# Kernel tuning notes

Measured on AMD Instinct MI355X. Metric: run time of the kernel, lower is better.

## Reference

```python
import jax, jax.numpy as jnp
import numpy as np

N_NODES = 50000
N_EDGES = 500000
DIM = 128
N_REL = 51
N_LAYERS = 4
B, K = 1024, 32
EPS = 1e-6


def setup_inputs() -> dict:
    key = jax.random.key(0)
    ks = jax.random.split(key, 10)
    x0 = jax.random.normal(ks[0], (N_NODES, DIM), jnp.float32)
    edge_index = jax.random.randint(ks[1], (2, N_EDGES), 0, N_NODES, dtype=jnp.int32)
    edge_type = jax.random.randint(ks[2], (N_EDGES,), 0, N_REL, dtype=jnp.int32)
    edge_weight = jnp.ones((N_EDGES,), jnp.float32)
    rel_w = jax.random.normal(ks[3], (N_LAYERS, N_REL, DIM), jnp.float32) * 0.1
    lin_w = jax.random.normal(ks[4], (N_LAYERS, 13 * DIM, DIM), jnp.float32) * (1.0 / np.sqrt(13 * DIM))
    lin_b = jnp.zeros((N_LAYERS, DIM), jnp.float32)
    ln_g = jnp.ones((N_LAYERS, DIM), jnp.float32)
    ln_b = jnp.zeros((N_LAYERS, DIM), jnp.float32)
    query_w = jax.random.normal(ks[5], (N_REL, DIM), jnp.float32) * 0.1
    src = jax.random.randint(ks[6], (B, K), 0, N_NODES, dtype=jnp.int32)
    rel = jax.random.randint(ks[7], (B, K), 0, N_REL, dtype=jnp.int32)
    dst = jax.random.randint(ks[8], (B, K), 0, N_NODES, dtype=jnp.int32)
    return dict(x0=x0, edge_index=edge_index, edge_type=edge_type, edge_weight=edge_weight,
                rel_w=rel_w, lin_w=lin_w, lin_b=lin_b, ln_g=ln_g, ln_b=ln_b,
                query_w=query_w, src=src, rel=rel, dst=dst)


def _rgcn_forward(x0, edge_weight, rel_w, lin_w, lin_b, ln_g, ln_b, query_w,
                  edge_index, edge_type, src, rel, dst):
    s, d = edge_index[0], edge_index[1]
    # in-degree (each node also gets an implicit boundary self-message)
    deg = jax.ops.segment_sum(jnp.ones((N_EDGES,), x0.dtype), d, num_segments=N_NODES)
    degree_out = deg[:, None] + 1.0  # [N,1]
    scale = jnp.log(degree_out)
    scale = scale / scale.mean()
    # PNA degree scalers: identity, amplification, attenuation  [N,3]
    scales = jnp.concatenate([jnp.ones_like(scale), scale, 1.0 / jnp.clip(scale, 1e-2)], axis=-1)

    x = x0
    for l in range(N_LAYERS):
        # distmult message per edge: [E, D]
        msg = x[s] * rel_w[l][edge_type] * edge_weight[:, None]
        # aggregate with boundary (x0) as self-loop message
        sum_m = jax.ops.segment_sum(msg, d, num_segments=N_NODES) + x0
        sum_sq = jax.ops.segment_sum(msg * msg, d, num_segments=N_NODES) + x0 * x0
        mx = jnp.maximum(jax.ops.segment_max(msg, d, num_segments=N_NODES), x0)
        mn = jnp.minimum(jax.ops.segment_min(msg, d, num_segments=N_NODES), x0)
        mean = sum_m / degree_out
        sq_mean = sum_sq / degree_out
        std = jnp.sqrt(jnp.clip(sq_mean - mean * mean, EPS, None))
        feats = jnp.stack([mean, mx, mn, std], axis=-2)        # [N,4,D]
        out = (feats[:, None, :, :] * scales[:, :, None, None]).reshape(N_NODES, 12 * DIM)
        out = jnp.concatenate([out, x], axis=-1) @ lin_w[l] + lin_b[l]  # [N,D]
        # layer norm
        mu = out.mean(-1, keepdims=True)
        var = out.var(-1, keepdims=True)
        out = (out - mu) / jnp.sqrt(var + 1e-5) * ln_g[l] + ln_b[l]
        out = jax.nn.relu(out)
        x = out + x  # short cut (same shapes)

    # distmult scoring over (src, rel, dst) triples: [B, K]
    return (x[src] * query_w[rel] * x[dst]).sum(-1)


def reference(x0, edge_index, edge_type, edge_weight, rel_w, lin_w, lin_b,
              ln_g, ln_b, query_w, src, rel, dst):
    return _rgcn_forward(x0, edge_weight, rel_w, lin_w, lin_b, ln_g, ln_b, query_w,
                         edge_index, edge_type, src, rel, dst)
```

## Files before the change

kernel.cpp:

```cpp
#include <hip/hip_runtime.h>
#include <math.h>

#define NNODES 50000
#define NEDGES 500000
#define DIM 128
#define NREL 51
#define NLAYERS 4
#define NTRIPLES (1024*32)
#define KDIM 1664
#define TILE_US 4096
#define NBLK 196

typedef float f2 __attribute__((ext_vector_type(2)));
typedef float f32x4 __attribute__((ext_vector_type(4)));
typedef short bf16x8 __attribute__((ext_vector_type(8)));

static __device__ __forceinline__ ushort bf16_rne(float v) {
  unsigned u = __float_as_uint(v);
  unsigned r = (u + 0x7fffu + ((u >> 16) & 1u)) >> 16;
  return (ushort)r;
}
static __device__ __forceinline__ float bf16_f(ushort h) {
  return __uint_as_float(((unsigned)h) << 16);
}
static __device__ __forceinline__ f2 unpack_bf2(uint u) {
  f2 r;
  r.x = __uint_as_float(u << 16);
  r.y = __uint_as_float(u & 0xffff0000u);
  return r;
}
static __device__ __forceinline__ f2 fmax2(f2 a, f2 b) { f2 r; r.x = fmaxf(a.x,b.x); r.y = fmaxf(a.y,b.y); return r; }
static __device__ __forceinline__ f2 fmin2(f2 a, f2 b) { f2 r; r.x = fminf(a.x,b.x); r.y = fminf(a.y,b.y); return r; }

static __device__ __forceinline__ void gload_lds16(const void* g, void* l) {
  __builtin_amdgcn_global_load_lds(
      (const __attribute__((address_space(1))) unsigned int*)g,
      (__attribute__((address_space(3))) unsigned int*)l,
      16, 0, 0);
}


__global__ void deg_hist_k(const int* __restrict__ ei, int* __restrict__ deg) {
  int e = blockIdx.x * blockDim.x + threadIdx.x;
  if (e < NEDGES) atomicAdd(&deg[ei[NEDGES + e]], 1);
}

__global__ void logsum_k(const int* __restrict__ deg, float* __restrict__ acc) {
  int i = blockIdx.x * blockDim.x + threadIdx.x;
  float v = (i < NNODES) ? logf((float)(deg[i] + 1)) : 0.0f;
  #pragma unroll
  for (int m = 32; m >= 1; m >>= 1) v += __shfl_xor(v, m, 64);
  __shared__ float ws[4];
  int lane = threadIdx.x & 63, w = threadIdx.x >> 6;
  if (lane == 0) ws[w] = v;
  __syncthreads();
  if (threadIdx.x == 0) atomicAdd(acc, ws[0] + ws[1] + ws[2] + ws[3]);
}


__global__ __launch_bounds__(256) void blocksum_k(const int* __restrict__ deg,
                                                  int* __restrict__ bsum) {
  int idx = blockIdx.x * 256 + threadIdx.x;
  int v = (idx < NNODES) ? deg[idx] : 0;
  #pragma unroll
  for (int m = 32; m >= 1; m >>= 1) v += __shfl_xor(v, m, 64);
  __shared__ int ws[4];
  int lane = threadIdx.x & 63, w = threadIdx.x >> 6;
  if (lane == 0) ws[w] = v;
  __syncthreads();
  if (threadIdx.x == 0) bsum[blockIdx.x] = ws[0] + ws[1] + ws[2] + ws[3];
}

__global__ __launch_bounds__(256) void bscan_k(const int* __restrict__ bsum,
                                               int* __restrict__ bofs) {
  int t = threadIdx.x;
  int v = (t < NBLK) ? bsum[t] : 0;
  int lane = t & 63, w = t >> 6;
  int sc = v;
  #pragma unroll
  for (int off = 1; off < 64; off <<= 1) {
    int u = __shfl_up(sc, off, 64);
    if (lane >= off) sc += u;
  }
  __shared__ int ws[4];
  if (lane == 63) ws[w] = sc;
  __syncthreads();
  int wo = 0;
  for (int i = 0; i < w; ++i) wo += ws[i];
  if (t < NBLK) bofs[t] = wo + sc - v;
}

__global__ __launch_bounds__(256) void csr_offsets_k(const int* __restrict__ deg,
                                                     const int* __restrict__ bofs,
                                                     int* __restrict__ row_start,
                                                     int* __restrict__ cursor) {
  int t = threadIdx.x;
  int idx = blockIdx.x * 256 + t;
  int v = (idx < NNODES) ? deg[idx] : 0;
  int lane = t & 63, w = t >> 6;
  int sc = v;
  #pragma unroll
  for (int off = 1; off < 64; off <<= 1) {
    int u = __shfl_up(sc, off, 64);
    if (lane >= off) sc += u;
  }
  __shared__ int ws[4];
  if (lane == 63) ws[w] = sc;
  __syncthreads();
  int wo = 0;
  for (int i = 0; i < w; ++i) wo += ws[i];
  int excl = bofs[blockIdx.x] + wo + sc - v;
  if (idx < NNODES) {
    row_start[idx] = excl;
    cursor[idx] = excl;
    if (idx == NNODES - 1) row_start[NNODES] = excl + v;
  }
}

__global__ void scales_k(const int* __restrict__ deg, const float* __restrict__ logsum,
                         float* __restrict__ scales) {
  int i = blockIdx.x * blockDim.x + threadIdx.x;
  if (i >= NNODES) return;
  float mean = *logsum / (float)NNODES;
  float sc = logf((float)(deg[i] + 1)) / mean;
  scales[i*3 + 0] = 1.0f;
  scales[i*3 + 1] = sc;
  scales[i*3 + 2] = 1.0f / fmaxf(sc, 0.01f);
}

__global__ void scatter_k(const int* __restrict__ ei, const int* __restrict__ etype,
                          const float* __restrict__ ew, int* __restrict__ cursor,
                          int* __restrict__ s_srt, int* __restrict__ t_srt,
                          float* __restrict__ w_srt) {
  int e = blockIdx.x * blockDim.x + threadIdx.x;
  if (e >= NEDGES) return;
  int d = ei[NEDGES + e];
  int pos = atomicAdd(&cursor[d], 1);
  s_srt[pos] = ei[e];
  t_srt[pos] = etype[e];
  w_srt[pos] = ew[e];
}


__global__ void wsplit_k(const float* __restrict__ W, ushort* __restrict__ wt) {
  int id = blockIdx.x * blockDim.x + threadIdx.x;
  if (id >= NLAYERS * KDIM * DIM) return;
  int col = id & 127;
  int k = (id >> 7) % KDIM;
  int l = id / (KDIM * DIM);
  float v = W[(size_t)l * KDIM * DIM + (size_t)k * DIM + col];
  ushort h = bf16_rne(v);
  ushort lo = bf16_rne(v - bf16_f(h));
  int c = k >> 5, kk = k & 31;
  int by = col >> 6, ch = col & 63;
  int tidx = (c < 48) ? ((c & 15) * 3 + (c >> 4)) : c;
  size_t base = (size_t)(((size_t)l * 2 + by) * 52 + tidx) * TILE_US;
  int slot = (kk >> 3) ^ ((ch >> 1) & 3);
  int off = ch * 32 + (slot << 3) + (kk & 7);
  wt[base + off] = h;
  wt[base + 2048 + off] = lo;
}


__global__ void xsplit_k(const float* __restrict__ x, ushort* __restrict__ xh,
                         ushort* __restrict__ xl) {
  int id = blockIdx.x * blockDim.x + threadIdx.x;
  if (id >= NNODES * 64) return;
  f2 v = *(const f2*)(x + (size_t)id * 2);
  ushort h0 = bf16_rne(v.x), h1 = bf16_rne(v.y);
  ushort l0 = bf16_rne(v.x - bf16_f(h0)), l1 = bf16_rne(v.y - bf16_f(h1));
  ((uint*)xh)[id] = (uint)h0 | ((uint)h1 << 16);
  ((uint*)xl)[id] = (uint)l0 | ((uint)l1 << 16);
}


__global__ __launch_bounds__(256) void aggregate_k(
    const ushort* __restrict__ xh, const float* __restrict__ x0,
    const float* __restrict__ relw, const int* __restrict__ row_start,
    const int* __restrict__ s_srt, const int* __restrict__ t_srt,
    const float* __restrict__ w_srt,
    ushort* __restrict__ sh)
{
  int wid = blockIdx.x * 4 + (threadIdx.x >> 6);
  if (wid >= NNODES) return;
  int lane = threadIdx.x & 63;
  int j0 = lane * 2;
  int beg = row_start[wid], end = row_start[wid + 1];
  int deg = end - beg;
  f2 sum = {0.f, 0.f}, sq = {0.f, 0.f};
  f2 mx = {-INFINITY, -INFINITY}, mn = {INFINITY, INFINITY};

  int eidx = beg + lane;
  bool va = eidx < end;
  int   sv = va ? s_srt[eidx] : 0;
  int   tv = va ? t_srt[eidx] : 0;
  float wv = va ? w_srt[eidx] : 0.0f;

  int n = (deg < 64) ? deg : 64;
  int e = 0;
  for (; e + 4 <= n; e += 4) {
    int s0 = __shfl(sv, e, 64),     s1 = __shfl(sv, e + 1, 64);
    int s2 = __shfl(sv, e + 2, 64), s3 = __shfl(sv, e + 3, 64);
    int t0 = __shfl(tv, e, 64),     t1 = __shfl(tv, e + 1, 64);
    int t2 = __shfl(tv, e + 2, 64), t3 = __shfl(tv, e + 3, 64);
    float w0 = __shfl(wv, e, 64),     w1 = __shfl(wv, e + 1, 64);
    float w2 = __shfl(wv, e + 2, 64), w3 = __shfl(wv, e + 3, 64);
    f2 xa = unpack_bf2(*(const uint*)(xh + (size_t)s0 * DIM + j0));
    f2 xb = unpack_bf2(*(const uint*)(xh + (size_t)s1 * DIM + j0));
    f2 xc = unpack_bf2(*(const uint*)(xh + (size_t)s2 * DIM + j0));
    f2 xd = unpack_bf2(*(const uint*)(xh + (size_t)s3 * DIM + j0));
    f2 ra = *(const f2*)(relw + (size_t)t0 * DIM + j0);
    f2 rb = *(const f2*)(relw + (size_t)t1 * DIM + j0);
    f2 rc = *(const f2*)(relw + (size_t)t2 * DIM + j0);
    f2 rd = *(const f2*)(relw + (size_t)t3 * DIM + j0);
    f2 m0 = xa * ra * w0;
    f2 m1 = xb * rb * w1;
    f2 m2 = xc * rc * w2;
    f2 m3 = xd * rd * w3;
    sum += m0 + m1 + m2 + m3;
    sq += m0*m0 + m1*m1 + m2*m2 + m3*m3;
    mx = fmax2(fmax2(fmax2(mx, m0), fmax2(m1, m2)), m3);
    mn = fmin2(fmin2(fmin2(mn, m0), fmin2(m1, m2)), m3);
  }
  for (; e < n; ++e) {
    int s = __shfl(sv, e, 64);
    int ty = __shfl(tv, e, 64);
    float w = __shfl(wv, e, 64);
    f2 xs = unpack_bf2(*(const uint*)(xh + (size_t)s * DIM + j0));
    f2 rv = *(const f2*)(relw + (size_t)ty * DIM + j0);
    f2 m = xs * rv * w;
    sum += m; sq += m * m;
    mx = fmax2(mx, m); mn = fmin2(mn, m);
  }
  for (int ee = beg + 64; ee < end; ++ee) {
    int s = s_srt[ee]; int ty = t_srt[ee]; float w = w_srt[ee];
    f2 xs = unpack_bf2(*(const uint*)(xh + (size_t)s * DIM + j0));
    f2 rv = *(const f2*)(relw + (size_t)ty * DIM + j0);
    f2 m = xs * rv * w;
    sum += m; sq += m * m;
    mx = fmax2(mx, m); mn = fmin2(mn, m);
  }

  f2 x0v = *(const f2*)(x0 + (size_t)wid * DIM + j0);
  sum += x0v; sq += x0v * x0v;
  mx = fmax2(mx, x0v); mn = fmin2(mn, x0v);
  float dq = (float)(deg + 1);
  f2 mean = sum / dq;
  f2 sqm = sq / dq;
  f2 var = sqm - mean * mean;
  f2 sd; sd.x = sqrtf(fmaxf(var.x, 1e-6f)); sd.y = sqrtf(fmaxf(var.y, 1e-6f));
  f2 feats[4] = {mean, mx, mn, sd};
  size_t base = (size_t)wid * 512 + j0;
  #pragma unroll
  for (int f = 0; f < 4; ++f) {
    f2 v = feats[f];
    ushort h0 = bf16_rne(v.x), h1 = bf16_rne(v.y);
    *(uint*)(sh + base + f * 128) = (uint)h0 | ((uint)h1 << 16);
  }
}


__global__ __launch_bounds__(512, 2) void gemm_mfma_k(
    const ushort* __restrict__ sh,
    const ushort* __restrict__ xh, const ushort* __restrict__ xl,
    const float* __restrict__ scales, const ushort* __restrict__ wtl,
    float* __restrict__ Y)
{
  __shared__ ushort As[2 * TILE_US];
  __shared__ ushort Bs[2][3 * TILE_US];
  int t = threadIdx.x;
  int w = t >> 6, lane = t & 63;
  int lr = lane & 15, lk = lane >> 4;
  int wr = w >> 1, wcq = w & 1;
  int row0 = blockIdx.x * 128;
  int by = blockIdx.y;

  int sr = t >> 2, sq = t & 3;
  int an = row0 + sr; if (an >= NNODES) an = NNODES - 1;
  int aoff = sr * 32 + ((sq ^ ((sr >> 1) & 3)) << 3);

  f32x4 p0_00, p0_01, p0_10, p0_11;
  f32x4 p1_00, p1_01, p1_10, p1_11;
  f32x4 p2_00, p2_01, p2_10, p2_11;
  p0_00 = p0_01 = p0_10 = p0_11 = (f32x4){0.f,0.f,0.f,0.f};
  p1_00 = p1_01 = p1_10 = p1_11 = (f32x4){0.f,0.f,0.f,0.f};
  p2_00 = p2_01 = p2_10 = p2_11 = (f32x4){0.f,0.f,0.f,0.f};

  bf16x8 rh, rl;
  auto loadA = [&](int cp) {
    if (cp < 16) {
      rh = *(const bf16x8*)(sh + (size_t)an * 512 + cp * 32 + sq * 8);
    } else {
      rh = *(const bf16x8*)(xh + (size_t)an * 128 + (cp - 16) * 32 + sq * 8);
      rl = *(const bf16x8*)(xl + (size_t)an * 128 + (cp - 16) * 32 + sq * 8);
    }
  };
  auto issueB = [&](int cp, ushort* dst) {
    int tile0 = (cp < 16) ? cp * 3 : cp + 32;
    const char* src = (const char*)(wtl + ((size_t)by * 52 + tile0) * TILE_US);
    char* d = (char*)dst;
    gload_lds16(src + t * 16, d + t * 16);
    if (cp < 16) {
      gload_lds16(src + (512 + t) * 16, d + (512 + t) * 16);
      gload_lds16(src + (1024 + t) * 16, d + (1024 + t) * 16);
    }
  };

  issueB(0, Bs[0]);
  loadA(0);
  *(bf16x8*)(As + aoff) = rh;
  __syncthreads();

  int cur = 0;
  const int ar = wr * 32 + lr;
  const int aswz = ar * 32 + ((lk ^ ((ar >> 1) & 3)) << 3);
  const int br = wcq * 32 + lr;
  const int bswz = br * 32 + ((lk ^ ((br >> 1) & 3)) << 3);

#define LOADB(Btile)                                                               \
    const ushort* Bb = (Btile) + bswz;                                             \
    bf16x8 bh0 = *(const bf16x8*)(Bb);                                             \
    bf16x8 bl0 = *(const bf16x8*)(Bb + 2048);                                      \
    bf16x8 bh1 = *(const bf16x8*)(Bb + 512);                                       \
    bf16x8 bl1 = *(const bf16x8*)(Bb + 2048 + 512);

#define MFMA_S2(pa, pb, pc, pd, Btile)                                             \
  {                                                                                \
    LOADB(Btile)                                                                   \
    pa = __builtin_amdgcn_mfma_f32_16x16x32_bf16(ah0, bh0, pa, 0,0,0);             \
    pa = __builtin_amdgcn_mfma_f32_16x16x32_bf16(ah0, bl0, pa, 0,0,0);             \
    pb = __builtin_amdgcn_mfma_f32_16x16x32_bf16(ah0, bh1, pb, 0,0,0);             \
    pb = __builtin_amdgcn_mfma_f32_16x16x32_bf16(ah0, bl1, pb, 0,0,0);             \
    pc = __builtin_amdgcn_mfma_f32_16x16x32_bf16(ah1, bh0, pc, 0,0,0);             \
    pc = __builtin_amdgcn_mfma_f32_16x16x32_bf16(ah1, bl0, pc, 0,0,0);             \
    pd = __builtin_amdgcn_mfma_f32_16x16x32_bf16(ah1, bh1, pd, 0,0,0);             \
    pd = __builtin_amdgcn_mfma_f32_16x16x32_bf16(ah1, bl1, pd, 0,0,0);             \
  }

#define MFMA_S3(pa, pb, pc, pd, Btile)                                             \
  {                                                                                \
    LOADB(Btile)                                                                   \
    pa = __builtin_amdgcn_mfma_f32_16x16x32_bf16(ah0, bh0, pa, 0,0,0);             \
    pa = __builtin_amdgcn_mfma_f32_16x16x32_bf16(ah0, bl0, pa, 0,0,0);             \
    pa = __builtin_amdgcn_mfma_f32_16x16x32_bf16(al0, bh0, pa, 0,0,0);             \
    pb = __builtin_amdgcn_mfma_f32_16x16x32_bf16(ah0, bh1, pb, 0,0,0);             \
    pb = __builtin_amdgcn_mfma_f32_16x16x32_bf16(ah0, bl1, pb, 0,0,0);             \
    pb = __builtin_amdgcn_mfma_f32_16x16x32_bf16(al0, bh1, pb, 0,0,0);             \
    pc = __builtin_amdgcn_mfma_f32_16x16x32_bf16(ah1, bh0, pc, 0,0,0);             \
    pc = __builtin_amdgcn_mfma_f32_16x16x32_bf16(ah1, bl0, pc, 0,0,0);             \
    pc = __builtin_amdgcn_mfma_f32_16x16x32_bf16(al1, bh0, pc, 0,0,0);             \
    pd = __builtin_amdgcn_mfma_f32_16x16x32_bf16(ah1, bh1, pd, 0,0,0);             \
    pd = __builtin_amdgcn_mfma_f32_16x16x32_bf16(ah1, bl1, pd, 0,0,0);             \
    pd = __builtin_amdgcn_mfma_f32_16x16x32_bf16(al1, bh1, pd, 0,0,0);             \
  }

  for (int cp = 0; cp < 20; ++cp) {
    if (cp < 19) {
      issueB(cp + 1, Bs[cur ^ 1]);
      loadA(cp + 1);
    }
    const ushort* Ab = As + aswz;
    const ushort* Bcur = Bs[cur];
    if (cp < 16) {
      bf16x8 ah0 = *(const bf16x8*)(Ab);
      bf16x8 ah1 = *(const bf16x8*)(Ab + 512);
      MFMA_S2(p0_00, p0_01, p0_10, p0_11, Bcur);
      MFMA_S2(p1_00, p1_01, p1_10, p1_11, Bcur + TILE_US);
      MFMA_S2(p2_00, p2_01, p2_10, p2_11, Bcur + 2 * TILE_US);
    } else {
      bf16x8 ah0 = *(const bf16x8*)(Ab);
      bf16x8 al0 = *(const bf16x8*)(Ab + TILE_US);
      bf16x8 ah1 = *(const bf16x8*)(Ab + 512);
      bf16x8 al1 = *(const bf16x8*)(Ab + TILE_US + 512);
      MFMA_S3(p0_00, p0_01, p0_10, p0_11, Bcur);
    }
    __syncthreads();
    if (cp < 19) {
      *(bf16x8*)(As + aoff) = rh;
      if (cp + 1 >= 16) *(bf16x8*)(As + TILE_US + aoff) = rl;
    }
    cur ^= 1;
    __syncthreads();
  }
#undef MFMA_S2
#undef MFMA_S3
#undef LOADB

  int colg = by * 64 + wcq * 32;
  f32x4 q0[2][2] = {{p0_00, p0_01}, {p0_10, p0_11}};
  f32x4 q1[2][2] = {{p1_00, p1_01}, {p1_10, p1_11}};
  f32x4 q2[2][2] = {{p2_00, p2_01}, {p2_10, p2_11}};
  #pragma unroll
  for (int fr = 0; fr < 2; ++fr) {
    int rbase = row0 + wr * 32 + fr * 16 + lk * 4;
    #pragma unroll
    for (int q = 0; q < 4; ++q) {
      int r = rbase + q;
      int rc = (r < NNODES) ? r : (NNODES - 1);
      float s1 = scales[rc * 3 + 1];
      float s2 = scales[rc * 3 + 2];
      if (r < NNODES) {
        #pragma unroll
        for (int fc = 0; fc < 2; ++fc) {
          float o = q0[fr][fc][q] + s1 * q1[fr][fc][q] + s2 * q2[fr][fc][q];
          Y[(size_t)r * DIM + colg + fc * 16 + lr] = o;
        }
      }
    }
  }
}


__global__ __launch_bounds__(256) void ln_k(
    const float* __restrict__ Y, const float* __restrict__ bias,
    const float* __restrict__ gam, const float* __restrict__ bet,
    float* __restrict__ x, ushort* __restrict__ xh, ushort* __restrict__ xl)
{
  int wid = blockIdx.x * 4 + (threadIdx.x >> 6);
  if (wid >= NNODES) return;
  int lane = threadIdx.x & 63;
  int j0 = lane * 2;
  f2 v = *(const f2*)(Y + (size_t)wid * DIM + j0);
  f2 b = *(const f2*)(bias + j0);
  v += b;
  float s = v.x + v.y;
  float q = v.x * v.x + v.y * v.y;
  #pragma unroll
  for (int m = 1; m < 64; m <<= 1) { s += __shfl_xor(s, m, 64); q += __shfl_xor(q, m, 64); }
  float mu = s * (1.0f / 128.0f);
  float var = q * (1.0f / 128.0f) - mu * mu;
  float rstd = rsqrtf(var + 1e-5f);
  f2 g = *(const f2*)(gam + j0);
  f2 be = *(const f2*)(bet + j0);
  f2 o = (v - mu) * rstd * g + be;
  o.x = fmaxf(o.x, 0.f); o.y = fmaxf(o.y, 0.f);
  float* xp = x + (size_t)wid * DIM + j0;
  f2 xr = *(const f2*)xp;
  f2 res = o + xr;
  *(f2*)xp = res;
  ushort h0 = bf16_rne(res.x), h1 = bf16_rne(res.y);
  ushort l0 = bf16_rne(res.x - bf16_f(h0)), l1 = bf16_rne(res.y - bf16_f(h1));
  *(uint*)(xh + (size_t)wid * 128 + j0) = (uint)h0 | ((uint)h1 << 16);
  *(uint*)(xl + (size_t)wid * 128 + j0) = (uint)l0 | ((uint)l1 << 16);
}


__global__ __launch_bounds__(256) void score_k(
    const float* __restrict__ x, const float* __restrict__ qw,
    const int* __restrict__ src, const int* __restrict__ rel,
    const int* __restrict__ dst, float* __restrict__ out)
{
  int wid = blockIdx.x * 4 + (threadIdx.x >> 6);
  if (wid >= NTRIPLES) return;
  int lane = threadIdx.x & 63;
  int j0 = lane * 2;
  int s = src[wid], r = rel[wid], d = dst[wid];
  f2 xs = *(const f2*)(x  + (size_t)s * DIM + j0);
  f2 q  = *(const f2*)(qw + (size_t)r * DIM + j0);
  f2 xd = *(const f2*)(x  + (size_t)d * DIM + j0);
  float p = xs.x*q.x*xd.x + xs.y*q.y*xd.y;
  #pragma unroll
  for (int m = 32; m >= 1; m >>= 1) p += __shfl_xor(p, m, 64);
  if (lane == 0) out[wid] = p;
}


extern "C" void kernel_launch(void* const* d_in, const int* in_sizes, int n_in,
                              void* d_out, int out_size, void* d_ws, size_t ws_size,
                              hipStream_t stream) {
  const float* x0    = (const float*)d_in[0];
  const int*   ei    = (const int*)d_in[1];
  const int*   etyp  = (const int*)d_in[2];
  const float* ew    = (const float*)d_in[3];
  const float* rel_w = (const float*)d_in[4];
  const float* lin_w = (const float*)d_in[5];
  const float* lin_b = (const float*)d_in[6];
  const float* ln_g  = (const float*)d_in[7];
  const float* lnb   = (const float*)d_in[8];
  const float* qw    = (const float*)d_in[9];
  const int*   srcq  = (const int*)d_in[10];
  const int*   relq  = (const int*)d_in[11];
  const int*   dstq  = (const int*)d_in[12];
  float* out = (float*)d_out;

  char* ws = (char*)d_ws;
  size_t off = 0;
  auto alloc = [&](size_t bytes) -> void* {
    void* p = ws + off; off = (off + bytes + 255) & ~(size_t)255; return p;
  };
  int*    deg       = (int*)alloc((size_t)NNODES * 4);
  int*    row_start = (int*)alloc((size_t)(NNODES + 1) * 4);
  int*    cursor    = (int*)alloc((size_t)NNODES * 4);
  int*    bsum      = (int*)alloc((size_t)(NBLK + 1) * 4);
  int*    bofs      = (int*)alloc((size_t)(NBLK + 1) * 4);
  int*    s_srt     = (int*)alloc((size_t)NEDGES * 4);
  int*    t_srt     = (int*)alloc((size_t)NEDGES * 4);
  float*  w_srt     = (float*)alloc((size_t)NEDGES * 4);
  float*  scales    = (float*)alloc((size_t)NNODES * 3 * 4);
  float*  logsum    = (float*)alloc(256);
  ushort* stats_hi  = (ushort*)alloc((size_t)NNODES * 512 * 2);
  float*  xbuf      = (float*)alloc((size_t)NNODES * DIM * 4);
  ushort* xhi       = (ushort*)alloc((size_t)NNODES * DIM * 2);
  ushort* xlo       = (ushort*)alloc((size_t)NNODES * DIM * 2);
  float*  Ybuf      = (float*)alloc((size_t)NNODES * DIM * 4);
  ushort* wtbuf     = (ushort*)alloc((size_t)NLAYERS * 2 * 52 * TILE_US * 2);

  hipMemsetAsync(deg, 0, (size_t)NNODES * 4, stream);
  hipMemsetAsync(logsum, 0, 4, stream);
  deg_hist_k<<<(NEDGES + 255) / 256, 256, 0, stream>>>(ei, deg);
  logsum_k<<<(NNODES + 255) / 256, 256, 0, stream>>>(deg, logsum);
  blocksum_k<<<NBLK, 256, 0, stream>>>(deg, bsum);
  bscan_k<<<1, 256, 0, stream>>>(bsum, bofs);
  csr_offsets_k<<<NBLK, 256, 0, stream>>>(deg, bofs, row_start, cursor);
  scales_k<<<(NNODES + 255) / 256, 256, 0, stream>>>(deg, logsum, scales);
  scatter_k<<<(NEDGES + 255) / 256, 256, 0, stream>>>(ei, etyp, ew, cursor, s_srt, t_srt, w_srt);
  wsplit_k<<<(NLAYERS * KDIM * DIM + 255) / 256, 256, 0, stream>>>(lin_w, wtbuf);
  hipMemcpyAsync(xbuf, x0, (size_t)NNODES * DIM * 4, hipMemcpyDeviceToDevice, stream);
  xsplit_k<<<(NNODES * 64 + 255) / 256, 256, 0, stream>>>(x0, xhi, xlo);

  for (int l = 0; l < NLAYERS; ++l) {
    aggregate_k<<<(NNODES + 3) / 4, 256, 0, stream>>>(
        xhi, x0, rel_w + (size_t)l * NREL * DIM, row_start, s_srt, t_srt, w_srt,
        stats_hi);
    dim3 gg((NNODES + 127) / 128, 2);
    gemm_mfma_k<<<gg, 512, 0, stream>>>(
        stats_hi, xhi, xlo, scales,
        wtbuf + (size_t)l * 2 * 52 * TILE_US, Ybuf);
    ln_k<<<(NNODES + 3) / 4, 256, 0, stream>>>(
        Ybuf, lin_b + (size_t)l * DIM, ln_g + (size_t)l * DIM, lnb + (size_t)l * DIM,
        xbuf, xhi, xlo);
  }
  score_k<<<(NTRIPLES + 3) / 4, 256, 0, stream>>>(xbuf, qw, srcq, relq, dstq, out);
}
```

Measured before the change: 569.4 us.

## Fuse layer norm into full-width GEMM and drop the Y round trip

The GEMM kernel now has each block own 64 rows across all 128 output columns. That lets it add the bias, stage the output tile in LDS, and apply layer norm, ReLU, the residual add and the bf16 hi/lo split in place. The separate ln_k launch and the fp32 Y buffer write and re-read go away. In exchange, the double-buffered B/A prefetch becomes a single buffer with two barriers per k-step, so global loads are no longer overlapped with MFMA work. The weight tile layout is also widened to 128 columns.

```diff
diff --git a/kernel.cpp b/kernel.cpp
--- a/kernel.cpp
+++ b/kernel.cpp
@@ -8,7 +8,7 @@
 #define NLAYERS 4
 #define NTRIPLES (1024*32)
 #define KDIM 1664
-#define TILE_US 4096
+#define TILE_US 8192
 #define NBLK 196
 
 typedef float f2 __attribute__((ext_vector_type(2)));
@@ -152,13 +152,12 @@
   ushort h = bf16_rne(v);
   ushort lo = bf16_rne(v - bf16_f(h));
   int c = k >> 5, kk = k & 31;
-  int by = col >> 6, ch = col & 63;
   int tidx = (c < 48) ? ((c & 15) * 3 + (c >> 4)) : c;
-  size_t base = (size_t)(((size_t)l * 2 + by) * 52 + tidx) * TILE_US;
-  int slot = (kk >> 3) ^ ((ch >> 1) & 3);
-  int off = ch * 32 + (slot << 3) + (kk & 7);
+  size_t base = (size_t)((size_t)l * 52 + tidx) * TILE_US;
+  int slot = (kk >> 3) ^ ((col >> 1) & 3);
+  int off = col * 32 + (slot << 3) + (kk & 7);
   wt[base + off] = h;
-  wt[base + 2048 + off] = lo;
+  wt[base + 4096 + off] = lo;
 }
 
 
@@ -260,22 +259,24 @@
 }
 
 
-__global__ __launch_bounds__(512, 2) void gemm_mfma_k(
+__global__ __launch_bounds__(512, 2) void gemm_fused_k(
     const ushort* __restrict__ sh,
     const ushort* __restrict__ xh, const ushort* __restrict__ xl,
     const float* __restrict__ scales, const ushort* __restrict__ wtl,
-    float* __restrict__ Y)
+    const float* __restrict__ bias, const float* __restrict__ gam,
+    const float* __restrict__ bet, float* __restrict__ x,
+    ushort* __restrict__ xho, ushort* __restrict__ xlo)
 {
-  __shared__ ushort As[2 * TILE_US];
-  __shared__ ushort Bs[2][3 * TILE_US];
+  __shared__ ushort As[2 * 2048];
+  __shared__ ushort Bs[3 * TILE_US];
   int t = threadIdx.x;
   int w = t >> 6, lane = t & 63;
   int lr = lane & 15, lk = lane >> 4;
-  int wr = w >> 1, wcq = w & 1;
-  int row0 = blockIdx.x * 128;
-  int by = blockIdx.y;
-
-  int sr = t >> 2, sq = t & 3;
+  int rg = w >> 2, cg = w & 3;
+  int row0 = blockIdx.x * 64;
+
+  int th = t & 255;
+  int sr = th >> 2, sq = th & 3;
   int an = row0 + sr; if (an >= NNODES) an = NNODES - 1;
   int aoff = sr * 32 + ((sq ^ ((sr >> 1) & 3)) << 3);
 
@@ -286,43 +287,44 @@
   p1_00 = p1_01 = p1_10 = p1_11 = (f32x4){0.f,0.f,0.f,0.f};
   p2_00 = p2_01 = p2_10 = p2_11 = (f32x4){0.f,0.f,0.f,0.f};
 
-  bf16x8 rh, rl;
+  bf16x8 rr;
   auto loadA = [&](int cp) {
-    if (cp < 16) {
-      rh = *(const bf16x8*)(sh + (size_t)an * 512 + cp * 32 + sq * 8);
-    } else {
-      rh = *(const bf16x8*)(xh + (size_t)an * 128 + (cp - 16) * 32 + sq * 8);
-      rl = *(const bf16x8*)(xl + (size_t)an * 128 + (cp - 16) * 32 + sq * 8);
+    if (t < 256) {
+      if (cp < 16) rr = *(const bf16x8*)(sh + (size_t)an * 512 + cp * 32 + sq * 8);
+      else         rr = *(const bf16x8*)(xh + (size_t)an * 128 + (cp - 16) * 32 + sq * 8);
+    } else if (cp >= 16) {
+      rr = *(const bf16x8*)(xl + (size_t)an * 128 + (cp - 16) * 32 + sq * 8);
     }
   };
-  auto issueB = [&](int cp, ushort* dst) {
+  auto writeA = [&](int cp) {
+    if (t < 256) *(bf16x8*)(As + aoff) = rr;
+    else if (cp >= 16) *(bf16x8*)(As + 2048 + aoff) = rr;
+  };
+  auto issueB = [&](int cp) {
     int tile0 = (cp < 16) ? cp * 3 : cp + 32;
-    const char* src = (const char*)(wtl + ((size_t)by * 52 + tile0) * TILE_US);
-    char* d = (char*)dst;
+    const char* src = (const char*)(wtl + (size_t)tile0 * TILE_US);
+    char* d = (char*)Bs;
     gload_lds16(src + t * 16, d + t * 16);
+    gload_lds16(src + (512 + t) * 16, d + (512 + t) * 16);
     if (cp < 16) {
-      gload_lds16(src + (512 + t) * 16, d + (512 + t) * 16);
       gload_lds16(src + (1024 + t) * 16, d + (1024 + t) * 16);
+      gload_lds16(src + (1536 + t) * 16, d + (1536 + t) * 16);
+      gload_lds16(src + (2048 + t) * 16, d + (2048 + t) * 16);
+      gload_lds16(src + (2560 + t) * 16, d + (2560 + t) * 16);
     }
   };
 
-  issueB(0, Bs[0]);
-  loadA(0);
-  *(bf16x8*)(As + aoff) = rh;
-  __syncthreads();
-
-  int cur = 0;
-  const int ar = wr * 32 + lr;
+  const int ar = rg * 32 + lr;
   const int aswz = ar * 32 + ((lk ^ ((ar >> 1) & 3)) << 3);
-  const int br = wcq * 32 + lr;
-  const int bswz = br * 32 + ((lk ^ ((br >> 1) & 3)) << 3);
+  const int bcol = cg * 32 + lr;
+  const int bswz = bcol * 32 + ((lk ^ ((bcol >> 1) & 3)) << 3);
 
 #define LOADB(Btile)                                                               \
     const ushort* Bb = (Btile) + bswz;                                             \
     bf16x8 bh0 = *(const bf16x8*)(Bb);                                             \
-    bf16x8 bl0 = *(const bf16x8*)(Bb + 2048);                                      \
+    bf16x8 bl0 = *(const bf16x8*)(Bb + 4096);                                      \
     bf16x8 bh1 = *(const bf16x8*)(Bb + 512);                                       \
-    bf16x8 bl1 = *(const bf16x8*)(Bb + 2048 + 512);
+    bf16x8 bl1 = *(const bf16x8*)(Bb + 4096 + 512);
 
 #define MFMA_S2(pa, pb, pc, pd, Btile)                                             \
   {                                                                                \
@@ -354,94 +356,86 @@
     pd = __builtin_amdgcn_mfma_f32_16x16x32_bf16(al1, bh1, pd, 0,0,0);             \
   }
 
+  loadA(0);
   for (int cp = 0; cp < 20; ++cp) {
-    if (cp < 19) {
-      issueB(cp + 1, Bs[cur ^ 1]);
-      loadA(cp + 1);
-    }
+    __syncthreads();
+    writeA(cp);
+    issueB(cp);
+    if (cp < 19) loadA(cp + 1);
+    __syncthreads();
     const ushort* Ab = As + aswz;
-    const ushort* Bcur = Bs[cur];
     if (cp < 16) {
       bf16x8 ah0 = *(const bf16x8*)(Ab);
       bf16x8 ah1 = *(const bf16x8*)(Ab + 512);
-      MFMA_S2(p0_00, p0_01, p0_10, p0_11, Bcur);
-      MFMA_S2(p1_00, p1_01, p1_10, p1_11, Bcur + TILE_US);
-      MFMA_S2(p2_00, p2_01, p2_10, p2_11, Bcur + 2 * TILE_US);
+      MFMA_S2(p0_00, p0_01, p0_10, p0_11, Bs);
+      MFMA_S2(p1_00, p1_01, p1_10, p1_11, Bs + TILE_US);
+      MFMA_S2(p2_00, p2_01, p2_10, p2_11, Bs + 2 * TILE_US);
     } else {
       bf16x8 ah0 = *(const bf16x8*)(Ab);
-      bf16x8 al0 = *(const bf16x8*)(Ab + TILE_US);
+      bf16x8 al0 = *(const bf16x8*)(Ab + 2048);
       bf16x8 ah1 = *(const bf16x8*)(Ab + 512);
-      bf16x8 al1 = *(const bf16x8*)(Ab + TILE_US + 512);
-      MFMA_S3(p0_00, p0_01, p0_10, p0_11, Bcur);
+      bf16x8 al1 = *(const bf16x8*)(Ab + 2048 + 512);
+      MFMA_S3(p0_00, p0_01, p0_10, p0_11, Bs);
     }
-    __syncthreads();
-    if (cp < 19) {
-      *(bf16x8*)(As + aoff) = rh;
-      if (cp + 1 >= 16) *(bf16x8*)(As + TILE_US + aoff) = rl;
-    }
-    cur ^= 1;
-    __syncthreads();
   }
 #undef MFMA_S2
 #undef MFMA_S3
 #undef LOADB
 
-  int colg = by * 64 + wcq * 32;
+  __syncthreads();
+  float* outT = (float*)Bs;
+  float bc0 = bias[cg * 32 + lr];
+  float bc1 = bias[cg * 32 + 16 + lr];
   f32x4 q0[2][2] = {{p0_00, p0_01}, {p0_10, p0_11}};
   f32x4 q1[2][2] = {{p1_00, p1_01}, {p1_10, p1_11}};
   f32x4 q2[2][2] = {{p2_00, p2_01}, {p2_10, p2_11}};
   #pragma unroll
   for (int fr = 0; fr < 2; ++fr) {
-    int rbase = row0 + wr * 32 + fr * 16 + lk * 4;
+    int lrbase = rg * 32 + fr * 16 + lk * 4;
     #pragma unroll
     for (int q = 0; q < 4; ++q) {
-      int r = rbase + q;
+      int lrow = lrbase + q;
+      int r = row0 + lrow;
       int rc = (r < NNODES) ? r : (NNODES - 1);
       float s1 = scales[rc * 3 + 1];
       float s2 = scales[rc * 3 + 2];
-      if (r < NNODES) {
-        #pragma unroll
-        for (int fc = 0; fc < 2; ++fc) {
-          float o = q0[fr][fc][q] + s1 * q1[fr][fc][q] + s2 * q2[fr][fc][q];
-          Y[(size_t)r * DIM + colg + fc * 16 + lr] = o;
-        }
-      }
+      outT[lrow * 132 + cg * 32 + lr] =
+          q0[fr][0][q] + s1 * q1[fr][0][q] + s2 * q2[fr][0][q] + bc0;
+      outT[lrow * 132 + cg * 32 + 16 + lr] =
+          q0[fr][1][q] + s1 * q1[fr][1][q] + s2 * q2[fr][1][q] + bc1;
     }
   }
-}
-
-
-__global__ __launch_bounds__(256) void ln_k(
-    const float* __restrict__ Y, const float* __restrict__ bias,
-    const float* __restrict__ gam, const float* __restrict__ bet,
-    float* __restrict__ x, ushort* __restrict__ xh, ushort* __restrict__ xl)
-{
-  int wid = blockIdx.x * 4 + (threadIdx.x >> 6);
-  if (wid >= NNODES) return;
-  int lane = threadIdx.x & 63;
+  __syncthreads();
+
   int j0 = lane * 2;
-  f2 v = *(const f2*)(Y + (size_t)wid * DIM + j0);
-  f2 b = *(const f2*)(bias + j0);
-  v += b;
-  float s = v.x + v.y;
-  float q = v.x * v.x + v.y * v.y;
-  #pragma unroll
-  for (int m = 1; m < 64; m <<= 1) { s += __shfl_xor(s, m, 64); q += __shfl_xor(q, m, 64); }
-  float mu = s * (1.0f / 128.0f);
-  float var = q * (1.0f / 128.0f) - mu * mu;
-  float rstd = rsqrtf(var + 1e-5f);
   f2 g = *(const f2*)(gam + j0);
   f2 be = *(const f2*)(bet + j0);
-  f2 o = (v - mu) * rstd * g + be;
-  o.x = fmaxf(o.x, 0.f); o.y = fmaxf(o.y, 0.f);
-  float* xp = x + (size_t)wid * DIM + j0;
-  f2 xr = *(const f2*)xp;
-  f2 res = o + xr;
-  *(f2*)xp = res;
-  ushort h0 = bf16_rne(res.x), h1 = bf16_rne(res.y);
-  ushort l0 = bf16_rne(res.x - bf16_f(h0)), l1 = bf16_rne(res.y - bf16_f(h1));
-  *(uint*)(xh + (size_t)wid * 128 + j0) = (uint)h0 | ((uint)h1 << 16);
-  *(uint*)(xl + (size_t)wid * 128 + j0) = (uint)l0 | ((uint)l1 << 16);
+  for (int rrow = 0; rrow < 8; ++rrow) {
+    int lrow = w * 8 + rrow;
+    int r = row0 + lrow;
+    f2 v;
+    v.x = outT[lrow * 132 + j0];
+    v.y = outT[lrow * 132 + j0 + 1];
+    float s = v.x + v.y;
+    float qq = v.x * v.x + v.y * v.y;
+    #pragma unroll
+    for (int m = 1; m < 64; m <<= 1) { s += __shfl_xor(s, m, 64); qq += __shfl_xor(qq, m, 64); }
+    float mu = s * (1.0f / 128.0f);
+    float var = qq * (1.0f / 128.0f) - mu * mu;
+    float rstd = rsqrtf(var + 1e-5f);
+    f2 o = (v - mu) * rstd * g + be;
+    o.x = fmaxf(o.x, 0.f); o.y = fmaxf(o.y, 0.f);
+    if (r < NNODES) {
+      float* xp = x + (size_t)r * DIM + j0;
+      f2 xr = *(const f2*)xp;
+      f2 res = o + xr;
+      *(f2*)xp = res;
+      ushort h0 = bf16_rne(res.x), h1 = bf16_rne(res.y);
+      ushort l0 = bf16_rne(res.x - bf16_f(h0)), l1 = bf16_rne(res.y - bf16_f(h1));
+      *(uint*)(xho + (size_t)r * DIM + j0) = (uint)h0 | ((uint)h1 << 16);
+      *(uint*)(xlo + (size_t)r * DIM + j0) = (uint)l0 | ((uint)l1 << 16);
+    }
+  }
 }
 
 
@@ -502,8 +496,7 @@
   float*  xbuf      = (float*)alloc((size_t)NNODES * DIM * 4);
   ushort* xhi       = (ushort*)alloc((size_t)NNODES * DIM * 2);
   ushort* xlo       = (ushort*)alloc((size_t)NNODES * DIM * 2);
-  float*  Ybuf      = (float*)alloc((size_t)NNODES * DIM * 4);
-  ushort* wtbuf     = (ushort*)alloc((size_t)NLAYERS * 2 * 52 * TILE_US * 2);
+  ushort* wtbuf     = (ushort*)alloc((size_t)NLAYERS * 52 * TILE_US * 2);
 
   hipMemsetAsync(deg, 0, (size_t)NNODES * 4, stream);
   hipMemsetAsync(logsum, 0, 4, stream);
@@ -522,12 +515,9 @@
     aggregate_k<<<(NNODES + 3) / 4, 256, 0, stream>>>(
         xhi, x0, rel_w + (size_t)l * NREL * DIM, row_start, s_srt, t_srt, w_srt,
         stats_hi);
-    dim3 gg((NNODES + 127) / 128, 2);
-    gemm_mfma_k<<<gg, 512, 0, stream>>>(
-        stats_hi, xhi, xlo, scales,
-        wtbuf + (size_t)l * 2 * 52 * TILE_US, Ybuf);
-    ln_k<<<(NNODES + 3) / 4, 256, 0, stream>>>(
-        Ybuf, lin_b + (size_t)l * DIM, ln_g + (size_t)l * DIM, lnb + (size_t)l * DIM,
+    gemm_fused_k<<<(NNODES + 63) / 64, 512, 0, stream>>>(
+        stats_hi, xhi, xlo, scales, wtbuf + (size_t)l * 52 * TILE_US,
+        lin_b + (size_t)l * DIM, ln_g + (size_t)l * DIM, lnb + (size_t)l * DIM,
         xbuf, xhi, xlo);
   }
   score_k<<<(NTRIPLES + 3) / 4, 256, 0, stream>>>(xbuf, qw, srcq, relq, dstq, out);
```

Result: faster. 550.1 us (-3.4%).
